# Performance work log

Measured on AMD Instinct MI355X. Metric: run time of the kernel, lower is better.

Reference implementation:

```python
import jax, jax.numpy as jnp
import numpy as np

E = 8       # expert_number
TOP_K = 2


def setup_inputs() -> dict:
    key = jax.random.key(0)
    ks = jax.random.split(key, 5)
    B, S, D, H = 4, 2048, 1024, 4096
    scale = 0.02
    return {
        "x": jax.random.normal(ks[0], (B, S, D), dtype=jnp.float32),
        "gate_w": jax.random.normal(ks[1], (D, E), dtype=jnp.float32) * scale,
        "gate_b": jnp.zeros((E,), dtype=jnp.float32),
        "w1": jax.random.normal(ks[2], (E, D, H), dtype=jnp.float32) * scale,
        "b1": jnp.zeros((E, H), dtype=jnp.float32),
        "w2": jax.random.normal(ks[3], (E, H, D), dtype=jnp.float32) * scale,
        "b2": jnp.zeros((E, D), dtype=jnp.float32),
    }


def reference(x, gate_w, gate_b, w1, b1, w2, b2):
    B, S, D = x.shape
    h = x.reshape(-1, D)                                   # [T, D]

    # Router: softmax in fp32, top-k, renormalize (matches torch code)
    router_logits = h @ gate_w + gate_b                    # [T, E]
    probs = jax.nn.softmax(router_logits.astype(jnp.float32), axis=-1)
    rw, sel = jax.lax.top_k(probs, TOP_K)                  # [T, K] each
    rw = rw / rw.sum(axis=-1, keepdims=True)
    rw = rw.astype(h.dtype)

    # Per-token combine weight for each expert (0 if not selected): [T, E]
    we = (jax.nn.one_hot(sel, E, dtype=h.dtype) * rw[..., None]).sum(axis=1)

    out = jnp.zeros_like(h)
    for e in range(E):  # fixed small expert count; per-expert GEMM + weighted combine
        mid = jax.nn.gelu(h @ w1[e] + b1[e], approximate=False)  # [T, H]
        ye = mid @ w2[e] + b2[e]                                 # [T, D]
        out = out + we[:, e:e + 1] * ye

    return out.reshape(B, S, D), router_logits
```

## Files before the change

kernel.cpp:

```cpp
#include <hip/hip_runtime.h>
#include <hip/hip_bf16.h>
#include <math.h>

#define T_TOKENS 8192
#define DDIM 1024
#define HDIM 4096
#define NEXP 8
#define CAP 8192
#define MAXTILES 136

typedef __bf16 bf16;
typedef __bf16 bf16x4 __attribute__((ext_vector_type(4)));
typedef __bf16 bf16x8 __attribute__((ext_vector_type(8)));
typedef float  floatx4 __attribute__((ext_vector_type(4)));

__device__ static inline void async_load16(const void* g, void* l)
{
    __builtin_amdgcn_global_load_lds(
        (const __attribute__((address_space(1))) void*)g,
        (__attribute__((address_space(3))) void*)l, 16, 0, 0);
}

__global__ void router_kernel(const float* __restrict__ x,
                              const float* __restrict__ gw,
                              const float* __restrict__ gbias,
                              float* __restrict__ logits_out,
                              int* counts, int* token_of,
                              int* selpack, int* slots, float* wts)
{
    int t = blockIdx.x * 4 + (threadIdx.x >> 6);
    int l = threadIdx.x & 63;
    const float4* xr = (const float4*)(x + (size_t)t * DDIM);

    float p[NEXP];
#pragma unroll
    for (int e = 0; e < NEXP; ++e) p[e] = 0.f;

#pragma unroll
    for (int it = 0; it < 4; ++it) {
        int d4 = it * 64 + l;
        float4 v = xr[d4];
        float vv[4] = {v.x, v.y, v.z, v.w};
#pragma unroll
        for (int j = 0; j < 4; ++j) {
            const float4* g4 = (const float4*)(gw + (size_t)(d4 * 4 + j) * NEXP);
            float4 ga = g4[0], gb4 = g4[1];
            p[0] += vv[j] * ga.x;  p[1] += vv[j] * ga.y;
            p[2] += vv[j] * ga.z;  p[3] += vv[j] * ga.w;
            p[4] += vv[j] * gb4.x; p[5] += vv[j] * gb4.y;
            p[6] += vv[j] * gb4.z; p[7] += vv[j] * gb4.w;
        }
    }
#pragma unroll
    for (int e = 0; e < NEXP; ++e) {
#pragma unroll
        for (int off = 32; off; off >>= 1) p[e] += __shfl_xor(p[e], off);
        p[e] += gbias[e];
    }
    if (l < NEXP) logits_out[(size_t)t * NEXP + l] = p[l];

    if (l == 0) {
        int e0 = 0;
#pragma unroll
        for (int e = 1; e < NEXP; ++e) if (p[e] > p[e0]) e0 = e;
        int e1 = -1;
#pragma unroll
        for (int e = 0; e < NEXP; ++e) {
            if (e == e0) continue;
            if (e1 < 0 || p[e] > p[e1]) e1 = e;
        }
        float w0 = 1.f / (1.f + expf(p[e1] - p[e0]));
        float w1 = 1.f / (1.f + expf(p[e0] - p[e1]));
        int s0 = atomicAdd(&counts[e0], 1);
        int s1 = atomicAdd(&counts[e1], 1);
        token_of[e0 * CAP + s0] = t;
        token_of[e1 * CAP + s1] = t;
        selpack[t] = e0 | (e1 << 8);
        slots[2 * t]     = s0;
        slots[2 * t + 1] = s1;
        wts[2 * t]     = w0;
        wts[2 * t + 1] = w1;
    }
}

__global__ void offsets_kernel(const int* __restrict__ counts,
                               int* __restrict__ offsets,
                               int* __restrict__ tiles)
{
    if (threadIdx.x == 0) {
        int tmp[MAXTILES];
        int a = 0, nt = 0;
        for (int e = 0; e < NEXP; ++e) {
            offsets[e] = a;
            for (int r = 0; r < counts[e]; r += 128)
                tmp[nt++] = (e << 24) | (a + r);
            a += counts[e];
        }
        offsets[NEXP] = a;
        int per = (nt + 7) >> 3;
        for (int p = 0; p < MAXTILES; ++p) {
            int c = p & 7, k = p >> 3;
            int src = c * per + k;
            tiles[p] = (k < per && src < nt) ? tmp[src] : -1;
        }
    }
}

__global__ void gather_kernel(const float* __restrict__ x,
                              const int* __restrict__ offsets,
                              const int* __restrict__ token_of,
                              bf16* __restrict__ xg)
{
    int row = blockIdx.x * 4 + (threadIdx.x >> 6);
    int l = threadIdx.x & 63;
    int e = 0;
#pragma unroll
    for (int i = 1; i < NEXP; ++i) e += (row >= offsets[i]);
    int t = token_of[e * CAP + (row - offsets[e])];
    const float4* src = (const float4*)(x + (size_t)t * DDIM);
    bf16x4* dst = (bf16x4*)(xg + (size_t)row * DDIM);
#pragma unroll
    for (int it = 0; it < 4; ++it) {
        float4 v = src[it * 64 + l];
        bf16x4 b;
        b[0] = (bf16)v.x; b[1] = (bf16)v.y; b[2] = (bf16)v.z; b[3] = (bf16)v.w;
        dst[it * 64 + l] = b;
    }
}

__global__ void transpose_cvt_kernel(const float* __restrict__ w1,
                                     const float* __restrict__ w2,
                                     bf16* __restrict__ w1b,
                                     bf16* __restrict__ w2b)
{
    __shared__ bf16 tile[64][68];
    int b = blockIdx.x;
    int R, C, e, tr, tc;
    const float* src;
    bf16* dst;
    if (b < 8192) {
        R = DDIM; C = HDIM;
        e = b >> 10; int tt = b & 1023;
        tc = tt & 63; tr = tt >> 6;
        src = w1 + (size_t)e * R * C; dst = w1b + (size_t)e * R * C;
    } else {
        b -= 8192;
        R = HDIM; C = DDIM;
        e = b >> 10; int tt = b & 1023;
        tc = tt & 15; tr = tt >> 4;
        src = w2 + (size_t)e * R * C; dst = w2b + (size_t)e * R * C;
    }
    int r0 = tr * 64, c0 = tc * 64;
    int t = threadIdx.x;
    int lr = t >> 4, c4 = t & 15;
#pragma unroll
    for (int it = 0; it < 4; ++it) {
        int r = lr + it * 16;
        float4 v = *(const float4*)(src + (size_t)(r0 + r) * C + c0 + c4 * 4);
        bf16x4 bb;
        bb[0] = (bf16)v.x; bb[1] = (bf16)v.y; bb[2] = (bf16)v.z; bb[3] = (bf16)v.w;
        *(bf16x4*)(&tile[r][c4 * 4]) = bb;
    }
    __syncthreads();
    int oc = t >> 3, rseg = (t & 7) * 8;
#pragma unroll
    for (int it = 0; it < 2; ++it) {
        int c = oc + it * 32;
        bf16x8 v;
#pragma unroll
        for (int j = 0; j < 8; ++j) v[j] = tile[rseg + j][c];
        *(bf16x8*)(dst + (size_t)(c0 + c) * R + r0 + rseg) = v;
    }
}

template<int KTOT>
__device__ static inline void stage_tile(const bf16* __restrict__ gbase,
                                         bf16* lds, int wave, int lane, int valid)
{
#pragma unroll
    for (int it = 0; it < 4; ++it) {
        int rbase = wave * 32 + it * 8;
        int rloc  = rbase + (lane >> 3);
        int grow  = rloc < valid ? rloc : (valid - 1);
        int chunk = (lane & 7) ^ (rloc & 7);
        const bf16* g = gbase + (size_t)grow * KTOT + chunk * 8;
        async_load16(g, lds + rbase * 64);
    }
}

__device__ static inline float fast_gelu(float v)
{
    float z = v * (2.302236479f + 0.1029451170f * v * v);
    float ex = __builtin_amdgcn_exp2f(z);
    return v * ex * __builtin_amdgcn_rcpf(ex + 1.f);
}

template<int KTOT, int NTOT, bool DOGELU, typename OutT>
__global__ __launch_bounds__(256, 4)
void moe_gemm(const bf16* __restrict__ Abase, const bf16* __restrict__ Bbase,
              const float* __restrict__ bias, OutT* __restrict__ Out,
              const int* __restrict__ tiles, const int* __restrict__ offsets)
{
    int info = tiles[blockIdx.x];
    if (info < 0) return;
    int e = info >> 24, row0 = info & 0xffffff;
    int valid = offsets[e + 1] - row0; if (valid > 128) valid = 128;
    int n0 = blockIdx.y * 128;

    const bf16* A = Abase + (size_t)row0 * KTOT;
    const bf16* B = Bbase + (size_t)e * NTOT * KTOT + (size_t)n0 * KTOT;
    const float* bvec = bias + (size_t)e * NTOT + n0;

    __shared__ __align__(16) bf16 As[128 * 64];
    __shared__ __align__(16) bf16 Bs[128 * 64];

    int tid = threadIdx.x;
    int lane = tid & 63, wave = tid >> 6;
    int wr = wave >> 1, wc = wave & 1;
    int m16 = lane & 15, quad = lane >> 4;
    int swz = m16 & 7;

    floatx4 acc[4][4];
#pragma unroll
    for (int i = 0; i < 4; ++i)
#pragma unroll
        for (int j = 0; j < 4; ++j)
#pragma unroll
            for (int r = 0; r < 4; ++r) acc[i][j][r] = 0.f;

    for (int k0 = 0; k0 < KTOT; k0 += 64) {
        stage_tile<KTOT>(A + k0, As, wave, lane, valid);
        stage_tile<KTOT>(B + k0, Bs, wave, lane, 128);
        __syncthreads();
#pragma unroll
        for (int ks = 0; ks < 64; ks += 32) {
            int cbase = (ks >> 3) + quad;
            int pchunk = (cbase ^ swz) * 8;
            bf16x8 af[4], bfr[4];
#pragma unroll
            for (int i = 0; i < 4; ++i)
                af[i] = *(const bf16x8*)(&As[(wr * 64 + i * 16 + m16) * 64 + pchunk]);
#pragma unroll
            for (int j = 0; j < 4; ++j)
                bfr[j] = *(const bf16x8*)(&Bs[(wc * 64 + j * 16 + m16) * 64 + pchunk]);
#pragma unroll
            for (int i = 0; i < 4; ++i)
#pragma unroll
                for (int j = 0; j < 4; ++j)
                    acc[i][j] = __builtin_amdgcn_mfma_f32_16x16x32_bf16(
                        af[i], bfr[j], acc[i][j], 0, 0, 0);
        }
        __syncthreads();
    }

#pragma unroll
    for (int i = 0; i < 4; ++i) {
#pragma unroll
        for (int r = 0; r < 4; ++r) {
            int lrow = wr * 64 + i * 16 + quad * 4 + r;
            if (lrow >= valid) continue;
            size_t orow = (size_t)(row0 + lrow) * NTOT + n0;
#pragma unroll
            for (int j = 0; j < 4; ++j) {
                int lcol = wc * 64 + j * 16 + m16;
                float v = acc[i][j][r] + bvec[lcol];
                if (DOGELU) v = fast_gelu(v);
                Out[orow + lcol] = (OutT)v;
            }
        }
    }
}

__global__ void combine_kernel(const float* __restrict__ y,
                               const int* __restrict__ offsets,
                               const int* __restrict__ selpack,
                               const int* __restrict__ slots,
                               const float* __restrict__ wts,
                               float* __restrict__ out)
{
    int t = blockIdx.x;
    int sp = selpack[t];
    int e0 = sp & 0xff, e1 = (sp >> 8) & 0xff;
    int p0 = offsets[e0] + slots[2 * t];
    int p1 = offsets[e1] + slots[2 * t + 1];
    float w0 = wts[2 * t], w1 = wts[2 * t + 1];
    const float4* y0 = (const float4*)(y + (size_t)p0 * DDIM);
    const float4* y1 = (const float4*)(y + (size_t)p1 * DDIM);
    float4* o = (float4*)(out + (size_t)t * DDIM);
    int tid = threadIdx.x;
    float4 a = y0[tid], b = y1[tid];
    float4 rr;
    rr.x = w0 * a.x + w1 * b.x;
    rr.y = w0 * a.y + w1 * b.y;
    rr.z = w0 * a.z + w1 * b.z;
    rr.w = w0 * a.w + w1 * b.w;
    o[tid] = rr;
}

extern "C" void kernel_launch(void* const* d_in, const int* in_sizes, int n_in,
                              void* d_out, int out_size, void* d_ws, size_t ws_size,
                              hipStream_t stream)
{
    (void)in_sizes; (void)n_in; (void)out_size; (void)ws_size;
    const float* x  = (const float*)d_in[0];
    const float* gw = (const float*)d_in[1];
    const float* gb = (const float*)d_in[2];
    const float* w1 = (const float*)d_in[3];
    const float* b1 = (const float*)d_in[4];
    const float* w2 = (const float*)d_in[5];
    const float* b2 = (const float*)d_in[6];
    float* out    = (float*)d_out;
    float* logits = out + (size_t)T_TOKENS * DDIM;

    char* ws = (char*)d_ws;
    const size_t MB = 1024 * 1024;
    int*   counts   = (int*)(ws + 0);
    int*   offsets  = (int*)(ws + 256);
    int*   tiles    = (int*)(ws + 512);
    int*   selpack  = (int*)(ws + 4096);
    int*   slots    = (int*)(ws + 4096 + 32 * 1024);
    float* wts      = (float*)(ws + 4096 + 96 * 1024);
    int*   token_of = (int*)(ws + 4096 + 160 * 1024);
    bf16*  xg  = (bf16*)(ws + 1 * MB);
    bf16*  w1b = (bf16*)(ws + 33 * MB);
    bf16*  w2b = (bf16*)(ws + 97 * MB);
    bf16*  mid = (bf16*)(ws + 161 * MB);
    float* y   = (float*)(ws + 289 * MB);

    hipMemsetAsync(counts, 0, 32, stream);

    router_kernel<<<T_TOKENS / 4, 256, 0, stream>>>(x, gw, gb, logits, counts,
                                                    token_of, selpack, slots, wts);
    offsets_kernel<<<1, 64, 0, stream>>>(counts, offsets, tiles);
    gather_kernel<<<2 * T_TOKENS / 4, 256, 0, stream>>>(x, offsets, token_of, xg);
    transpose_cvt_kernel<<<16384, 256, 0, stream>>>(w1, w2, w1b, w2b);
    moe_gemm<DDIM, HDIM, true, bf16><<<dim3(MAXTILES, HDIM / 128), 256, 0, stream>>>(
        xg, w1b, b1, mid, tiles, offsets);
    moe_gemm<HDIM, DDIM, false, float><<<dim3(MAXTILES, DDIM / 128), 256, 0, stream>>>(
        mid, w2b, b2, y, tiles, offsets);
    combine_kernel<<<T_TOKENS, 256, 0, stream>>>(y, offsets, selpack, slots, wts, out);
}
```

Baseline: 956.4 us.

## Rewrite MoE grouped GEMM with 256x256 tiles and 4-stage async LDS pipeline

The grouped expert GEMM moves from 128x128 tiles with 256 threads and a single-buffered K=64 loop to 256x256 tiles with 512 threads (8 waves). It uses a 4-deep ring of K=32 LDS buffers fed by async global-to-LDS loads, interleaved with MFMA phases, wave priority hints and split barriers. The offsets kernel is parallelised and now emits 256-row tiles. The goal is to hide global-load latency behind MFMA work and to raise arithmetic intensity per block. The cost is higher register pressure, fewer blocks (72x16 and 72x4), and more padding waste on partially filled expert tiles.

After: 963.8 us. Within noise of the previous version (+0.8%).

```diff
diff --git a/kernel.cpp b/kernel.cpp
--- a/kernel.cpp
+++ b/kernel.cpp
@@ -7,7 +7,7 @@
 #define HDIM 4096
 #define NEXP 8
 #define CAP 8192
-#define MAXTILES 136
+#define MAXTILES 72
 
 typedef __bf16 bf16;
 typedef __bf16 bf16x4 __attribute__((ext_vector_type(4)));
@@ -87,22 +87,33 @@
                                int* __restrict__ offsets,
                                int* __restrict__ tiles)
 {
-    if (threadIdx.x == 0) {
-        int tmp[MAXTILES];
+    __shared__ int off[NEXP + 1], tstart[NEXP + 1];
+    int t = threadIdx.x;
+    if (t == 0) {
         int a = 0, nt = 0;
         for (int e = 0; e < NEXP; ++e) {
-            offsets[e] = a;
-            for (int r = 0; r < counts[e]; r += 128)
-                tmp[nt++] = (e << 24) | (a + r);
-            a += counts[e];
-        }
-        offsets[NEXP] = a;
-        int per = (nt + 7) >> 3;
-        for (int p = 0; p < MAXTILES; ++p) {
-            int c = p & 7, k = p >> 3;
-            int src = c * per + k;
-            tiles[p] = (k < per && src < nt) ? tmp[src] : -1;
-        }
+            off[e] = a; tstart[e] = nt;
+            int c = counts[e];
+            a += c; nt += (c + 255) >> 8;
+        }
+        off[NEXP] = a;
+        tstart[NEXP] = nt;
+    }
+    __syncthreads();
+    if (t <= NEXP) offsets[t] = off[t];
+    int nt = tstart[NEXP];
+    int per = (nt + 7) >> 3;
+    if (t < MAXTILES) {
+        int c = t & 7, k = t >> 3;
+        int src = c * per + k;
+        int v = -1;
+        if (k < per && src < nt) {
+            int e = 0;
+#pragma unroll
+            for (int i = 1; i < NEXP; ++i) e += (src >= tstart[i]);
+            v = (e << 24) | (off[e] + (src - tstart[e]) * 256);
+        }
+        tiles[t] = v;
     }
 }
 
@@ -173,21 +184,6 @@
     }
 }
 
-template<int KTOT>
-__device__ static inline void stage_tile(const bf16* __restrict__ gbase,
-                                         bf16* lds, int wave, int lane, int valid)
-{
-#pragma unroll
-    for (int it = 0; it < 4; ++it) {
-        int rbase = wave * 32 + it * 8;
-        int rloc  = rbase + (lane >> 3);
-        int grow  = rloc < valid ? rloc : (valid - 1);
-        int chunk = (lane & 7) ^ (rloc & 7);
-        const bf16* g = gbase + (size_t)grow * KTOT + chunk * 8;
-        async_load16(g, lds + rbase * 64);
-    }
-}
-
 __device__ static inline float fast_gelu(float v)
 {
     float z = v * (2.302236479f + 0.1029451170f * v * v);
@@ -196,74 +192,125 @@
 }
 
 template<int KTOT, int NTOT, bool DOGELU, typename OutT>
-__global__ __launch_bounds__(256, 4)
+__global__ __launch_bounds__(512, 2)
 void moe_gemm(const bf16* __restrict__ Abase, const bf16* __restrict__ Bbase,
               const float* __restrict__ bias, OutT* __restrict__ Out,
               const int* __restrict__ tiles, const int* __restrict__ offsets)
 {
+    constexpr int NK = KTOT / 32;
+    __shared__ __align__(16) bf16 lds[4 * 2 * 256 * 32];
+
     int info = tiles[blockIdx.x];
     if (info < 0) return;
     int e = info >> 24, row0 = info & 0xffffff;
-    int valid = offsets[e + 1] - row0; if (valid > 128) valid = 128;
-    int n0 = blockIdx.y * 128;
+    int valid = offsets[e + 1] - row0; if (valid > 256) valid = 256;
+    int n0 = blockIdx.y * 256;
 
     const bf16* A = Abase + (size_t)row0 * KTOT;
     const bf16* B = Bbase + (size_t)e * NTOT * KTOT + (size_t)n0 * KTOT;
     const float* bvec = bias + (size_t)e * NTOT + n0;
 
-    __shared__ __align__(16) bf16 As[128 * 64];
-    __shared__ __align__(16) bf16 Bs[128 * 64];
-
     int tid = threadIdx.x;
     int lane = tid & 63, wave = tid >> 6;
-    int wr = wave >> 1, wc = wave & 1;
+    int wm = wave >> 2, wn = wave & 3;
     int m16 = lane & 15, quad = lane >> 4;
-    int swz = m16 & 7;
-
-    floatx4 acc[4][4];
-#pragma unroll
-    for (int i = 0; i < 4; ++i)
-#pragma unroll
-        for (int j = 0; j < 4; ++j)
-#pragma unroll
-            for (int r = 0; r < 4; ++r) acc[i][j][r] = 0.f;
-
-    for (int k0 = 0; k0 < KTOT; k0 += 64) {
-        stage_tile<KTOT>(A + k0, As, wave, lane, valid);
-        stage_tile<KTOT>(B + k0, Bs, wave, lane, 128);
-        __syncthreads();
-#pragma unroll
-        for (int ks = 0; ks < 64; ks += 32) {
-            int cbase = (ks >> 3) + quad;
-            int pchunk = (cbase ^ swz) * 8;
-            bf16x8 af[4], bfr[4];
-#pragma unroll
-            for (int i = 0; i < 4; ++i)
-                af[i] = *(const bf16x8*)(&As[(wr * 64 + i * 16 + m16) * 64 + pchunk]);
-#pragma unroll
-            for (int j = 0; j < 4; ++j)
-                bfr[j] = *(const bf16x8*)(&Bs[(wc * 64 + j * 16 + m16) * 64 + pchunk]);
-#pragma unroll
-            for (int i = 0; i < 4; ++i)
-#pragma unroll
-                for (int j = 0; j < 4; ++j)
-                    acc[i][j] = __builtin_amdgcn_mfma_f32_16x16x32_bf16(
-                        af[i], bfr[j], acc[i][j], 0, 0, 0);
-        }
-        __syncthreads();
-    }
-
-#pragma unroll
-    for (int i = 0; i < 4; ++i) {
+    int pcb = (quad ^ ((m16 >> 1) & 3)) * 8;
+
+    int rowoff = lane >> 2;
+    int clog = (lane & 3) ^ ((lane >> 3) & 3);
+
+    int ar0 = wave * 16 + rowoff;
+    int ar1 = 128 + wave * 16 + rowoff;
+    const bf16* gA0 = A + (size_t)(ar0 < valid ? ar0 : valid - 1) * KTOT + clog * 8;
+    const bf16* gA1 = A + (size_t)(ar1 < valid ? ar1 : valid - 1) * KTOT + clog * 8;
+    const bf16* gB0 = B + (size_t)ar0 * KTOT + clog * 8;
+    const bf16* gB1 = B + (size_t)ar1 * KTOT + clog * 8;
+
+    int ldsW0 = wave * 16 * 32;
+    int ldsW1 = (128 + wave * 16) * 32;
+
+    floatx4 acc[8][4];
+#pragma unroll
+    for (int m = 0; m < 8; ++m)
+#pragma unroll
+        for (int n = 0; n < 4; ++n)
+#pragma unroll
+            for (int r = 0; r < 4; ++r) acc[m][n][r] = 0.f;
+
+#pragma unroll
+    for (int pt = 0; pt < 3; ++pt) {
+        bf16* bufA = lds + pt * 16384;
+        bf16* bufB = bufA + 8192;
+        async_load16(gA0 + pt * 32, bufA + ldsW0);
+        async_load16(gA1 + pt * 32, bufA + ldsW1);
+        async_load16(gB0 + pt * 32, bufB + ldsW0);
+        async_load16(gB1 + pt * 32, bufB + ldsW1);
+    }
+    asm volatile("s_waitcnt vmcnt(8)" ::: "memory");
+    __builtin_amdgcn_s_barrier();
+    __builtin_amdgcn_sched_barrier(0);
+
+    for (int t = 0; t < NK; ++t) {
+        const bf16* As = lds + (t & 3) * 16384;
+        const bf16* Bs = As + 8192;
+        int s = t + 3; if (s > NK - 1) s = NK - 1;
+        bf16* stA = lds + ((t + 3) & 3) * 16384;
+        bf16* stB = stA + 8192;
+
+        bf16x8 bfr[4], af[4];
+#pragma unroll
+        for (int n = 0; n < 4; ++n)
+            bfr[n] = *(const bf16x8*)(&Bs[(wn * 64 + n * 16 + m16) * 32 + pcb]);
+#pragma unroll
+        for (int m = 0; m < 4; ++m)
+            af[m] = *(const bf16x8*)(&As[(wm * 128 + m * 16 + m16) * 32 + pcb]);
+        async_load16(gA0 + s * 32, stA + ldsW0);
+        async_load16(gA1 + s * 32, stA + ldsW1);
+        __builtin_amdgcn_s_barrier();
+        __builtin_amdgcn_sched_barrier(0);
+        __builtin_amdgcn_s_setprio(1);
+#pragma unroll
+        for (int m = 0; m < 4; ++m)
+#pragma unroll
+            for (int n = 0; n < 4; ++n)
+                acc[m][n] = __builtin_amdgcn_mfma_f32_16x16x32_bf16(
+                    af[m], bfr[n], acc[m][n], 0, 0, 0);
+        __builtin_amdgcn_s_setprio(0);
+        __builtin_amdgcn_s_barrier();
+        __builtin_amdgcn_sched_barrier(0);
+
+        bf16x8 ag[4];
+#pragma unroll
+        for (int m = 0; m < 4; ++m)
+            ag[m] = *(const bf16x8*)(&As[(wm * 128 + (m + 4) * 16 + m16) * 32 + pcb]);
+        async_load16(gB0 + s * 32, stB + ldsW0);
+        async_load16(gB1 + s * 32, stB + ldsW1);
+        __builtin_amdgcn_s_barrier();
+        __builtin_amdgcn_sched_barrier(0);
+        __builtin_amdgcn_s_setprio(1);
+#pragma unroll
+        for (int m = 0; m < 4; ++m)
+#pragma unroll
+            for (int n = 0; n < 4; ++n)
+                acc[m + 4][n] = __builtin_amdgcn_mfma_f32_16x16x32_bf16(
+                    ag[m], bfr[n], acc[m + 4][n], 0, 0, 0);
+        __builtin_amdgcn_s_setprio(0);
+        asm volatile("s_waitcnt vmcnt(8)" ::: "memory");
+        __builtin_amdgcn_s_barrier();
+        __builtin_amdgcn_sched_barrier(0);
+    }
+
+#pragma unroll
+    for (int m = 0; m < 8; ++m) {
 #pragma unroll
         for (int r = 0; r < 4; ++r) {
-            int lrow = wr * 64 + i * 16 + quad * 4 + r;
+            int lrow = wm * 128 + m * 16 + quad * 4 + r;
             if (lrow >= valid) continue;
             size_t orow = (size_t)(row0 + lrow) * NTOT + n0;
 #pragma unroll
-            for (int j = 0; j < 4; ++j) {
-                int lcol = wc * 64 + j * 16 + m16;
-                float v = acc[i][j][r] + bvec[lcol];
+            for (int n = 0; n < 4; ++n) {
+                int lcol = wn * 64 + n * 16 + m16;
+                float v = acc[m][n][r] + bvec[lcol];
                 if (DOGELU) v = fast_gelu(v);
                 Out[orow + lcol] = (OutT)v;
             }
@@ -331,12 +378,12 @@
 
     router_kernel<<<T_TOKENS / 4, 256, 0, stream>>>(x, gw, gb, logits, counts,
                                                     token_of, selpack, slots, wts);
-    offsets_kernel<<<1, 64, 0, stream>>>(counts, offsets, tiles);
+    offsets_kernel<<<1, 128, 0, stream>>>(counts, offsets, tiles);
     gather_kernel<<<2 * T_TOKENS / 4, 256, 0, stream>>>(x, offsets, token_of, xg);
     transpose_cvt_kernel<<<16384, 256, 0, stream>>>(w1, w2, w1b, w2b);
-    moe_gemm<DDIM, HDIM, true, bf16><<<dim3(MAXTILES, HDIM / 128), 256, 0, stream>>>(
+    moe_gemm<DDIM, HDIM, true, bf16><<<dim3(MAXTILES, HDIM / 256), 512, 0, stream>>>(
         xg, w1b, b1, mid, tiles, offsets);
-    moe_gemm<HDIM, DDIM, false, float><<<dim3(MAXTILES, DDIM / 128), 256, 0, stream>>>(
+    moe_gemm<HDIM, DDIM, false, float><<<dim3(MAXTILES, DDIM / 256), 512, 0, stream>>>(
         mid, w2b, b2, y, tiles, offsets);
     combine_kernel<<<T_TOKENS, 256, 0, stream>>>(y, offsets, selpack, slots, wts, out);
 }
```
